# Performance work log

Measured on AMD Instinct MI355X. Metric: run time of the kernel, lower is better.

## Reference

```python
import jax, jax.numpy as jnp
import numpy as np

N = 100000   # nodes
E = 1600000  # edges per meta-path graph
D_IN = 256
H = 4        # num_heads
F = 32       # out_feats per head
D_HID = H * F  # 128
D_SEM = 128  # semantic attention hidden dim
C = 8        # output classes
NEG_SLOPE = 0.2


def setup_inputs() -> dict:
    key = jax.random.key(0)
    ks = jax.random.split(key, 24)
    inp = {
        "x": jax.random.normal(ks[0], (N, D_IN), dtype=jnp.float32),
        "src0": jax.random.randint(ks[1], (E,), 0, N),
        "dst0": jax.random.randint(ks[2], (E,), 0, N),
        "ew0": jax.random.uniform(ks[3], (E,), dtype=jnp.float32),
        "src1": jax.random.randint(ks[4], (E,), 0, N),
        "dst1": jax.random.randint(ks[5], (E,), 0, N),
        "ew1": jax.random.uniform(ks[6], (E,), dtype=jnp.float32),
    }
    s_in = 1.0 / np.sqrt(D_IN)
    s_f = 1.0 / np.sqrt(F)
    s_h = 1.0 / np.sqrt(D_HID)
    s_s = 1.0 / np.sqrt(D_SEM)
    # GAT params for meta-path 0 and 1 (tuple feat -> separate fc_src/fc_dst)
    inp["Wsrc0"] = jax.random.normal(ks[7], (D_IN, D_HID), dtype=jnp.float32) * s_in
    inp["Wdst0"] = jax.random.normal(ks[8], (D_IN, D_HID), dtype=jnp.float32) * s_in
    inp["al0"] = jax.random.normal(ks[9], (H, F), dtype=jnp.float32) * s_f
    inp["ar0"] = jax.random.normal(ks[10], (H, F), dtype=jnp.float32) * s_f
    inp["b0"] = jnp.zeros((D_HID,), dtype=jnp.float32)
    inp["Wsrc1"] = jax.random.normal(ks[11], (D_IN, D_HID), dtype=jnp.float32) * s_in
    inp["Wdst1"] = jax.random.normal(ks[12], (D_IN, D_HID), dtype=jnp.float32) * s_in
    inp["al1"] = jax.random.normal(ks[13], (H, F), dtype=jnp.float32) * s_f
    inp["ar1"] = jax.random.normal(ks[14], (H, F), dtype=jnp.float32) * s_f
    inp["b1"] = jnp.zeros((D_HID,), dtype=jnp.float32)
    # Semantic attention: Linear(D_HID->128) -> tanh -> Linear(128->1, no bias)
    inp["Wp1"] = jax.random.normal(ks[15], (D_HID, D_SEM), dtype=jnp.float32) * s_h
    inp["bp1"] = jnp.zeros((D_SEM,), dtype=jnp.float32)
    inp["Wp2"] = jax.random.normal(ks[16], (D_SEM, 1), dtype=jnp.float32) * s_s
    # Prediction head
    inp["Wo"] = jax.random.normal(ks[17], (D_HID, C), dtype=jnp.float32) * s_h
    inp["bo"] = jnp.zeros((C,), dtype=jnp.float32)
    return inp


def gat_conv(x, Wsrc, Wdst, al, ar, b, src, dst, ew):
    # feat_src/feat_dst: [N, H, F]
    fs = (x @ Wsrc).reshape(N, H, F)
    fd = (x @ Wdst).reshape(N, H, F)
    el = jnp.einsum('nhf,hf->nh', fs, al)  # [N, H]
    er = jnp.einsum('nhf,hf->nh', fd, ar)  # [N, H]
    e = jax.nn.leaky_relu(el[src] + er[dst], negative_slope=NEG_SLOPE)  # [E, H]
    a = jax.nn.sigmoid(e) * ew[:, None]  # [E, H]  (sigmoid attention * edge_weight)
    m = fs[src] * a[:, :, None]  # [E, H, F]
    out = jax.ops.segment_sum(m, dst, num_segments=N)  # [N, H, F]
    out = out + b.reshape(1, H, F)
    return jax.nn.elu(out).reshape(N, H * F)


def semantic_attention(z, Wp1, bp1, Wp2):
    # z: [N, P, D_HID]
    w = jnp.tanh(z @ Wp1 + bp1) @ Wp2  # [N, P, 1]
    w = w.mean(axis=0)                  # [P, 1]
    beta = jax.nn.softmax(w, axis=0)    # softmax over meta-paths
    return (beta[None] * z).sum(axis=1)  # [N, D_HID]


def reference(x, src0, dst0, ew0, src1, dst1, ew1,
              Wsrc0, Wdst0, al0, ar0, b0,
              Wsrc1, Wdst1, al1, ar1, b1,
              Wp1, bp1, Wp2, Wo, bo):
    z0 = gat_conv(x, Wsrc0, Wdst0, al0, ar0, b0, src0, dst0, ew0)
    z1 = gat_conv(x, Wsrc1, Wdst1, al1, ar1, b1, src1, dst1, ew1)
    z = jnp.stack([z0, z1], axis=1)  # [N, 2, H*F]
    h = semantic_attention(z, Wp1, bp1, Wp2)  # [N, H*F]
    return h @ Wo + bo  # [N, C]
```

## Files before the change

kernel.cpp:

```cpp
#include <hip/hip_runtime.h>
#include <hip/hip_fp16.h>
#include <math.h>

#define N_NODES 100000
#define N_EDGES 1600000
#define D_IN    256
#define D_HID   128
#define NH      4
#define NF      32
#define D_SEM   128
#define NC      8
#define NEG_SLOPE 0.2f
#define BUCKET  64
#define BIN_SHIFT 8
#define BINS    391
#define BIN_CAP 4608
#define CHUNK   4096

typedef _Float16 half8 __attribute__((ext_vector_type(8)));
typedef float    floatx4 __attribute__((ext_vector_type(4)));

__global__ void prep_fold(const float* __restrict__ Ws0, const float* __restrict__ al0,
                          const float* __restrict__ Wd0, const float* __restrict__ ar0,
                          const float* __restrict__ Ws1, const float* __restrict__ al1,
                          const float* __restrict__ Wd1, const float* __restrict__ ar1,
                          float* __restrict__ WF) {
    int d = threadIdx.x;
    for (int p = 0; p < 2; ++p) {
        const float* Ws = p ? Ws1 : Ws0;
        const float* al = p ? al1 : al0;
        const float* Wd = p ? Wd1 : Wd0;
        const float* ar = p ? ar1 : ar0;
        for (int h = 0; h < NH; ++h) {
            float se = 0.f, sr = 0.f;
            for (int f = 0; f < NF; ++f) {
                se = fmaf(Ws[d*D_HID + h*NF + f], al[h*NF + f], se);
                sr = fmaf(Wd[d*D_HID + h*NF + f], ar[h*NF + f], sr);
            }
            WF[d*16 + p*8 + h]     = se;
            WF[d*16 + p*8 + 4 + h] = sr;
        }
    }
}

__global__ __launch_bounds__(256) void prep_tr(const float* __restrict__ Ws0,
                                               const float* __restrict__ Ws1,
                                               const float* __restrict__ Wp1,
                                               __half* __restrict__ WT0,
                                               __half* __restrict__ WT1,
                                               __half* __restrict__ WP1T) {
    int g = blockIdx.x * 256 + threadIdx.x;
    if (g < 32768) {
        int c = g >> 8, k = g & 255;
        WT0[g] = __float2half_rn(Ws0[k*D_HID + c]);
    } else if (g < 65536) {
        int g2 = g - 32768;
        int c = g2 >> 8, k = g2 & 255;
        WT1[g2] = __float2half_rn(Ws1[k*D_HID + c]);
    } else {
        int g2 = g - 65536;
        int c = g2 >> 7, k = g2 & 127;
        WP1T[g2] = __float2half_rn(Wp1[k*D_SEM + c]);
    }
}

__global__ __launch_bounds__(256) void er_el_kernel(const float* __restrict__ x,
                                                    const float* __restrict__ WF,
                                                    float* __restrict__ eler,
                                                    __half* __restrict__ XH) {
    __shared__ float xs[16][260];
    __shared__ float wfs[4096];
    int tid = threadIdx.x;
    #pragma unroll
    for (int i = 0; i < 16; ++i) wfs[tid + i*256] = WF[tid + i*256];
    int n0 = blockIdx.x * 16;
    #pragma unroll
    for (int i = 0; i < 4; ++i) {
        int id = tid + i*256;
        int r = id >> 6, c = (id & 63) << 2;
        *(float4*)&xs[r][c] = *(const float4*)&x[(size_t)(n0 + r)*D_IN + c];
    }
    __syncthreads();
    int node = tid >> 4, c = tid & 15;
    float s = 0.f;
    #pragma unroll 8
    for (int k = 0; k < 256; ++k) s = fmaf(xs[node][k], wfs[k*16 + c], s);
    int p = c >> 3, e = (c >> 2) & 1, h = c & 3;
    eler[(p*2 + e)*400000 + (n0 + node)*4 + h] = s;

    #pragma unroll
    for (int i = 0; i < 4; ++i) {
        int id = tid + i*256;
        int r = id >> 6, c4 = (id & 63) << 2;
        float4 v = *(const float4*)&xs[r][c4];
        __half2 h0 = __floats2half2_rn(v.x, v.y);
        __half2 h1 = __floats2half2_rn(v.z, v.w);
        uint2 pk; pk.x = *(unsigned*)&h0; pk.y = *(unsigned*)&h1;
        *(uint2*)&XH[(size_t)(n0 + r)*D_IN + c4] = pk;
    }
}

__global__ __launch_bounds__(256) void gemm_fs_mfma(const __half* __restrict__ XH,
                                                    const __half* __restrict__ WT,
                                                    __half* __restrict__ FS) {
    __shared__ unsigned short xs[64][64];
    __shared__ unsigned short ws[128][64];
    int tid = threadIdx.x;
    int row0 = blockIdx.x * 64;
    int wid = tid >> 6, lane = tid & 63;
    int wm = wid >> 1, wn = wid & 1;
    int lr = lane & 15, lk = lane >> 4;

    floatx4 acc[2][4];
    #pragma unroll
    for (int m = 0; m < 2; ++m)
        #pragma unroll
        for (int n = 0; n < 4; ++n) acc[m][n] = (floatx4){0.f, 0.f, 0.f, 0.f};

    for (int k0 = 0; k0 < D_IN; k0 += 64) {
        #pragma unroll
        for (int i = 0; i < 2; ++i) {
            int id = tid + i*256;
            int r = id >> 3, c8 = (id & 7) << 3;
            int grow = row0 + r;
            uint4 pk = make_uint4(0u, 0u, 0u, 0u);
            if (grow < N_NODES) pk = *(const uint4*)&XH[(size_t)grow*D_IN + k0 + c8];
            int cc = (((c8 >> 3) ^ (r & 7)) << 3);
            *(uint4*)&xs[r][cc] = pk;
        }
        #pragma unroll
        for (int i = 0; i < 8; ++i) {
            int id = tid + i*256;
            int col = id >> 4, c4 = (id & 15) << 2;
            uint2 pk = *(const uint2*)&WT[col*256 + k0 + c4];
            int cc = (((c4 >> 3) ^ (col & 7)) << 3) + (c4 & 7);
            *(uint2*)&ws[col][cc] = pk;
        }
        __syncthreads();
        #pragma unroll
        for (int kk = 0; kk < 2; ++kk) {
            int ksub = kk*4 + lk;
            half8 a[2], b[4];
            #pragma unroll
            for (int m = 0; m < 2; ++m) {
                int r = wm*32 + m*16 + lr;
                a[m] = *(half8*)&xs[r][((ksub ^ (r & 7)) << 3)];
            }
            #pragma unroll
            for (int n = 0; n < 4; ++n) {
                int c = wn*64 + n*16 + lr;
                b[n] = *(half8*)&ws[c][((ksub ^ (c & 7)) << 3)];
            }
            #pragma unroll
            for (int m = 0; m < 2; ++m)
                #pragma unroll
                for (int n = 0; n < 4; ++n)
                    acc[m][n] = __builtin_amdgcn_mfma_f32_16x16x32_f16(a[m], b[n], acc[m][n], 0, 0, 0);
        }
        __syncthreads();
    }

    unsigned short* outs = &ws[0][0];
    #pragma unroll
    for (int m = 0; m < 2; ++m)
        #pragma unroll
        for (int n = 0; n < 4; ++n) {
            int col = wn*64 + n*16 + lr;
            #pragma unroll
            for (int r4 = 0; r4 < 4; ++r4) {
                int rr = wm*32 + m*16 + lk*4 + r4;
                __half hv = __float2half_rn(acc[m][n][r4]);
                outs[rr*128 + col] = *(unsigned short*)&hv;
            }
        }
    __syncthreads();
    #pragma unroll
    for (int i = 0; i < 8; ++i) {
        int id = tid + i*256;
        int r = id >> 5, c4 = (id & 31) << 2;
        int grow = row0 + r;
        if (grow < N_NODES)
            *(uint2*)&FS[(size_t)grow*D_HID + c4] = *(uint2*)&outs[r*128 + c4];
    }
}

__global__ __launch_bounds__(1024) void bin_kernel(const int* __restrict__ src,
                                                   const int* __restrict__ dst,
                                                   const float* __restrict__ ew,
                                                   int* __restrict__ gcur,
                                                   uint2* __restrict__ binned) {
    __shared__ uint2 stage[CHUNK];
    __shared__ unsigned short binof[CHUNK];
    __shared__ int bcnt[512], boff[512], gbase[512], brun[512];
    int tid = threadIdx.x;
    int c0 = blockIdx.x * CHUNK;
    int C = N_EDGES - c0; if (C > CHUNK) C = CHUNK;
    if (C <= 0) return;

    if (tid < 512) bcnt[tid] = 0;
    __syncthreads();
    for (int j = tid; j < C; j += 1024)
        atomicAdd(&bcnt[dst[c0 + j] >> BIN_SHIFT], 1);
    __syncthreads();

    int v = (tid < 512) ? bcnt[tid] : 0;
    if (tid < 512) boff[tid] = v;
    __syncthreads();
    for (int o = 1; o < 512; o <<= 1) {
        int u = (tid < 512 && tid >= o) ? boff[tid - o] : 0;
        __syncthreads();
        if (tid < 512) boff[tid] += u;
        __syncthreads();
    }
    if (tid < 512) {
        boff[tid] -= v;
        brun[tid] = 0;
        if (tid < BINS) gbase[tid] = v ? atomicAdd(&gcur[tid], v) : 0;
    }
    __syncthreads();

    for (int j = tid; j < C; j += 1024) {
        int e = c0 + j;
        int d = dst[e];
        int b = d >> BIN_SHIFT;
        unsigned q = (unsigned)(ew[e] * 32767.f + 0.5f);
        int p = atomicAdd(&brun[b], 1);
        int sl = boff[b] + p;
        stage[sl] = make_uint2(((unsigned)src[e] << 15) | q, (unsigned)d);
        binof[sl] = (unsigned short)b;
    }
    __syncthreads();

    for (int j = tid; j < C; j += 1024) {
        int b = binof[j];
        int off = gbase[b] + (j - boff[b]);
        if (off < BIN_CAP) binned[b * BIN_CAP + off] = stage[j];
    }
}

__global__ __launch_bounds__(1024) void bucket_kernel(const int* __restrict__ gcur,
                                                      const uint2* __restrict__ binned,
                                                      int* __restrict__ cnt,
                                                      unsigned* __restrict__ edg) {
    __shared__ unsigned buck[256 * BUCKET];
    __shared__ int lcnt[256];
    int tid = threadIdx.x;
    int b = blockIdx.x;
    int n0 = b << BIN_SHIFT;
    if (tid < 256) lcnt[tid] = 0;
    __syncthreads();

    int cE = gcur[b]; if (cE > BIN_CAP) cE = BIN_CAP;
    for (int j = tid; j < cE; j += 1024) {
        uint2 r = binned[b * BIN_CAP + j];
        int dl = (int)r.y - n0;
        int p = atomicAdd(&lcnt[dl], 1);
        if (p < BUCKET) buck[(dl << 6) + p] = r.x;
    }
    __syncthreads();

    const uint4* b4 = (const uint4*)buck;
    uint4* e4 = (uint4*)edg;
    for (int i = tid; i < 256 * BUCKET / 4; i += 1024) {
        int node = n0 + (i >> 4);
        int used = lcnt[i >> 4];
        if (node < N_NODES && ((i & 15) << 2) < used)
            e4[((size_t)node << 4) + (i & 15)] = b4[i];
    }
    if (tid < 256) {
        int node = n0 + tid;
        if (node < N_NODES) cnt[node] = lcnt[tid] < BUCKET ? lcnt[tid] : BUCKET;
    }
}

__device__ __forceinline__ float sel4(float4 v, int h) {
    float ab = (h & 1) ? v.y : v.x;
    float cd = (h & 1) ? v.w : v.z;
    return (h & 2) ? cd : ab;
}
__device__ __forceinline__ float coef_of(unsigned w, float v) {
    float a = (float)(w & 32767u) * (1.f / 32767.f);
    v = v > 0.f ? v : NEG_SLOPE * v;
    return a * __builtin_amdgcn_rcpf(1.f + __expf(-v));
}

__global__ __launch_bounds__(256) void agg_kernel(const __half* __restrict__ FS,
                                                  const float* __restrict__ el,
                                                  const float* __restrict__ er,
                                                  const int* __restrict__ cnt,
                                                  const unsigned* __restrict__ edg,
                                                  const float* __restrict__ bias,
                                                  __half* __restrict__ zh) {
    int wv = (blockIdx.x * 256 + threadIdx.x) >> 6;
    int lane = threadIdx.x & 63;
    if (wv >= N_NODES) return;
    int q   = lane >> 4;
    int ql  = lane & 15;
    int hh  = lane & 3;
    int eL  = lane >> 2;
    int cn = cnt[wv];
    if (cn > BUCKET) cn = BUCKET;
    int beg = wv << 6;
    const __half* fsq = FS + (ql << 3);

    unsigned w0 = 0, w1 = 0, w2 = 0, w3 = 0;
    if (eL      < cn) w0 = edg[beg + eL];
    if (eL + 16 < cn) w1 = edg[beg + 16 + eL];
    if (eL + 32 < cn) w2 = edg[beg + 32 + eL];
    if (eL + 48 < cn) w3 = edg[beg + 48 + eL];
    int s0v = (int)(w0 >> 15), s1v = (int)(w1 >> 15);
    int s2v = (int)(w2 >> 15), s3v = (int)(w3 >> 15);
    float4 el0 = *(const float4*)&el[s0v*4];
    float4 el1 = *(const float4*)&el[s1v*4];
    float4 el2 = *(const float4*)&el[s2v*4];
    float4 el3 = *(const float4*)&el[s3v*4];
    float erh = sel4(*(const float4*)&er[wv*4], hh);
    float c0v = (eL      < cn) ? coef_of(w0, sel4(el0, hh) + erh) : 0.f;
    float c1v = (eL + 16 < cn) ? coef_of(w1, sel4(el1, hh) + erh) : 0.f;
    float c2v = (eL + 32 < cn) ? coef_of(w2, sel4(el2, hh) + erh) : 0.f;
    float c3v = (eL + 48 < cn) ? coef_of(w3, sel4(el3, hh) + erh) : 0.f;

    float4 a0 = make_float4(0.f,0.f,0.f,0.f);
    float4 a1 = make_float4(0.f,0.f,0.f,0.f);
    int qsh = q << 2, hsel = ql >> 2;

#define AGG_PHASE(SP, CP, BASE)                                               \
    if ((BASE) < cn) {                                                        \
        _Pragma("unroll")                                                     \
        for (int u = 0; u < 4; ++u) {                                         \
            int lsrc = (u << 4) | qsh;                                        \
            int ssrc = __shfl(SP, lsrc);                                      \
            float av = __shfl(CP, lsrc | hsel);                               \
            uint4 raw = make_uint4(0u,0u,0u,0u);                              \
            if ((BASE) + (u << 2) + q < cn)                                   \
                raw = *(const uint4*)&fsq[(size_t)ssrc * D_HID];              \
            float2 f0 = __half22float2(*(__half2*)&raw.x);                    \
            float2 f1 = __half22float2(*(__half2*)&raw.y);                    \
            float2 f2 = __half22float2(*(__half2*)&raw.z);                    \
            float2 f3 = __half22float2(*(__half2*)&raw.w);                    \
            a0.x = fmaf(f0.x, av, a0.x); a0.y = fmaf(f0.y, av, a0.y);         \
            a0.z = fmaf(f1.x, av, a0.z); a0.w = fmaf(f1.y, av, a0.w);         \
            a1.x = fmaf(f2.x, av, a1.x); a1.y = fmaf(f2.y, av, a1.y);         \
            a1.z = fmaf(f3.x, av, a1.z); a1.w = fmaf(f3.y, av, a1.w);         \
        }                                                                     \
    }
    AGG_PHASE(s0v, c0v, 0)
    AGG_PHASE(s1v, c1v, 16)
    AGG_PHASE(s2v, c2v, 32)
    AGG_PHASE(s3v, c3v, 48)
#undef AGG_PHASE

    #pragma unroll
    for (int o = 16; o < 64; o <<= 1) {
        a0.x += __shfl_xor(a0.x, o); a0.y += __shfl_xor(a0.y, o);
        a0.z += __shfl_xor(a0.z, o); a0.w += __shfl_xor(a0.w, o);
        a1.x += __shfl_xor(a1.x, o); a1.y += __shfl_xor(a1.y, o);
        a1.z += __shfl_xor(a1.z, o); a1.w += __shfl_xor(a1.w, o);
    }

    if (q < 2) {
        int c = (ql << 3) + (q << 2);
        float4 r = q ? a1 : a0;
        float4 bv = *(const float4*)&bias[c];
        r.x += bv.x; r.y += bv.y; r.z += bv.z; r.w += bv.w;
        r.x = r.x > 0.f ? r.x : expm1f(r.x);
        r.y = r.y > 0.f ? r.y : expm1f(r.y);
        r.z = r.z > 0.f ? r.z : expm1f(r.z);
        r.w = r.w > 0.f ? r.w : expm1f(r.w);
        __half2 h0 = __floats2half2_rn(r.x, r.y);
        __half2 h1 = __floats2half2_rn(r.z, r.w);
        uint2 pk; pk.x = *(unsigned*)&h0; pk.y = *(unsigned*)&h1;
        *(uint2*)&zh[(size_t)wv*D_HID + c] = pk;
    }
}

__global__ __launch_bounds__(256) void sem_mfma(const __half* __restrict__ zh0,
                                                const __half* __restrict__ zh1,
                                                const __half* __restrict__ WP1T,
                                                const float* __restrict__ bp1,
                                                const float* __restrict__ Wp2,
                                                float* __restrict__ wsum) {
    __shared__ unsigned short zs[64][128];
    __shared__ unsigned short ps[128][128];
    __shared__ float red[4];
    const __half* z = blockIdx.y ? zh1 : zh0;
    int tid = threadIdx.x;
    int row0 = blockIdx.x * 64;
    int wid = tid >> 6, lane = tid & 63;
    int wm = wid >> 1, wn = wid & 1;
    int lr = lane & 15, lk = lane >> 4;

    #pragma unroll
    for (int i = 0; i < 4; ++i) {
        int id = tid + i*256;
        int r = id >> 4, ch = id & 15;
        int grow = row0 + r;
        uint4 pk = make_uint4(0u, 0u, 0u, 0u);
        if (grow < N_NODES) pk = *(const uint4*)&z[(size_t)grow*D_HID + (ch << 3)];
        *(uint4*)&zs[r][((ch ^ (r & 7)) << 3)] = pk;
    }
    #pragma unroll
    for (int i = 0; i < 16; ++i) {
        int id = tid + i*256;
        int c = id >> 5, k4 = (id & 31) << 2;
        uint2 pk = *(const uint2*)&WP1T[c*128 + k4];
        int cc = (((k4 >> 3) ^ (c & 7)) << 3) + (k4 & 7);
        *(uint2*)&ps[c][cc] = pk;
    }
    __syncthreads();

    floatx4 acc[2][4];
    #pragma unroll
    for (int m = 0; m < 2; ++m)
        #pragma unroll
        for (int n = 0; n < 4; ++n) acc[m][n] = (floatx4){0.f, 0.f, 0.f, 0.f};

    #pragma unroll
    for (int kk = 0; kk < 4; ++kk) {
        int ksub = kk*4 + lk;
        half8 a[2], b[4];
        #pragma unroll
        for (int m = 0; m < 2; ++m) {
            int r = wm*32 + m*16 + lr;
            a[m] = *(half8*)&zs[r][((ksub ^ (r & 7)) << 3)];
        }
        #pragma unroll
        for (int n = 0; n < 4; ++n) {
            int c = wn*64 + n*16 + lr;
            b[n] = *(half8*)&ps[c][((ksub ^ (c & 7)) << 3)];
        }
        #pragma unroll
        for (int m = 0; m < 2; ++m)
            #pragma unroll
            for (int n = 0; n < 4; ++n)
                acc[m][n] = __builtin_amdgcn_mfma_f32_16x16x32_f16(a[m], b[n], acc[m][n], 0, 0, 0);
    }

    float s = 0.f;
    #pragma unroll
    for (int m = 0; m < 2; ++m)
        #pragma unroll
        for (int n = 0; n < 4; ++n) {
            int col = wn*64 + n*16 + lr;
            float bp = bp1[col];
            float w2 = Wp2[col];
            #pragma unroll
            for (int r4 = 0; r4 < 4; ++r4) {
                int grow = row0 + wm*32 + m*16 + lk*4 + r4;
                if (grow < N_NODES) {
                    float v = acc[m][n][r4] + bp;
                    float t = 1.f - 2.f / (__expf(2.f*v) + 1.f);
                    s = fmaf(t, w2, s);
                }
            }
        }
    #pragma unroll
    for (int o = 1; o < 64; o <<= 1) s += __shfl_xor(s, o);
    if (lane == 0) red[wid] = s;
    __syncthreads();
    if (tid == 0) atomicAdd(&wsum[blockIdx.y], red[0] + red[1] + red[2] + red[3]);
}

__global__ __launch_bounds__(256) void final_kernel(const __half* __restrict__ zh0,
                                                    const __half* __restrict__ zh1,
                                                    const float* __restrict__ Wo,
                                                    const float* __restrict__ bo,
                                                    const float* __restrict__ wsum,
                                                    float* __restrict__ out) {
    __shared__ float z0s[32][132];
    __shared__ float z1s[32][132];
    __shared__ float wos[128*8];
    __shared__ float bos[8];
    int tid = threadIdx.x;
    int n0 = blockIdx.x * 32;
    #pragma unroll
    for (int i = 0; i < 4; ++i) wos[tid + i*256] = Wo[tid + i*256];
    if (tid < 8) bos[tid] = bo[tid];
    #pragma unroll
    for (int i = 0; i < 2; ++i) {
        int id = tid + i*256;
        int r = id >> 4, c8 = (id & 15) << 3;
        uint4 p0 = *(const uint4*)&zh0[(size_t)(n0 + r)*D_HID + c8];
        uint4 p1 = *(const uint4*)&zh1[(size_t)(n0 + r)*D_HID + c8];
        float2 q0 = __half22float2(*(__half2*)&p0.x);
        float2 q1 = __half22float2(*(__half2*)&p0.y);
        float2 q2 = __half22float2(*(__half2*)&p0.z);
        float2 q3 = __half22float2(*(__half2*)&p0.w);
        *(float4*)&z0s[r][c8]     = make_float4(q0.x, q0.y, q1.x, q1.y);
        *(float4*)&z0s[r][c8 + 4] = make_float4(q2.x, q2.y, q3.x, q3.y);
        q0 = __half22float2(*(__half2*)&p1.x);
        q1 = __half22float2(*(__half2*)&p1.y);
        q2 = __half22float2(*(__half2*)&p1.z);
        q3 = __half22float2(*(__half2*)&p1.w);
        *(float4*)&z1s[r][c8]     = make_float4(q0.x, q0.y, q1.x, q1.y);
        *(float4*)&z1s[r][c8 + 4] = make_float4(q2.x, q2.y, q3.x, q3.y);
    }
    __syncthreads();

    float w0 = wsum[0] * (1.f / N_NODES), w1 = wsum[1] * (1.f / N_NODES);
    float m = fmaxf(w0, w1);
    float e0 = __expf(w0 - m), e1 = __expf(w1 - m);
    float b0 = e0 / (e0 + e1), b1 = 1.f - b0;

    int node = tid >> 3, c = tid & 7;
    float s = bos[c];
    #pragma unroll 8
    for (int k = 0; k < 128; ++k) {
        float hk = b0 * z0s[node][k] + b1 * z1s[node][k];
        s = fmaf(hk, wos[k*8 + c], s);
    }
    out[(n0 + node)*NC + c] = s;
}

extern "C" void kernel_launch(void* const* d_in, const int* in_sizes, int n_in,
                              void* d_out, int out_size, void* d_ws, size_t ws_size,
                              hipStream_t stream) {
    const float* x     = (const float*)d_in[0];
    const int*   src0  = (const int*)  d_in[1];
    const int*   dst0  = (const int*)  d_in[2];
    const float* ew0   = (const float*)d_in[3];
    const int*   src1  = (const int*)  d_in[4];
    const int*   dst1  = (const int*)  d_in[5];
    const float* ew1   = (const float*)d_in[6];
    const float* Wsrc0 = (const float*)d_in[7];
    const float* Wdst0 = (const float*)d_in[8];
    const float* al0   = (const float*)d_in[9];
    const float* ar0   = (const float*)d_in[10];
    const float* b0    = (const float*)d_in[11];
    const float* Wsrc1 = (const float*)d_in[12];
    const float* Wdst1 = (const float*)d_in[13];
    const float* al1   = (const float*)d_in[14];
    const float* ar1   = (const float*)d_in[15];
    const float* b1    = (const float*)d_in[16];
    const float* Wp1   = (const float*)d_in[17];
    const float* bp1   = (const float*)d_in[18];
    const float* Wp2   = (const float*)d_in[19];
    const float* Wo    = (const float*)d_in[20];
    const float* bo    = (const float*)d_in[21];
    float* out = (float*)d_out;

    float*    ws     = (float*)d_ws;
    __half*   FS     = (__half*)ws;
    __half*   ZH0    = (__half*)(ws + 6400000);
    __half*   ZH1    = (__half*)(ws + 12800000);
    __half*   XH     = (__half*)(ws + 19200000);
    float*    ELER   = ws + 32000000;
    float*    WF     = ELER + 1600000;
    float*    WSUM   = WF + 4096;
    __half*   WT0    = (__half*)(WSUM + 8);
    __half*   WT1    = (__half*)((float*)WT0 + 16384);
    __half*   WP1T   = (__half*)((float*)WT1 + 16384);
    int*      CNT0   = (int*)((float*)WP1T + 8192);
    int*      CNT1   = CNT0  + 100000;
    int*      GCUR0  = CNT1  + 100000;
    int*      GCUR1  = GCUR0 + 512;
    unsigned* EDG    = (unsigned*)(GCUR1 + 512);
    uint2*    BINNED = (uint2*)(EDG + 6400000);

    hipMemsetAsync(GCUR0, 0, sizeof(int)*1024, stream);
    hipMemsetAsync(WSUM, 0, sizeof(float)*4, stream);

    prep_fold<<<1, 256, 0, stream>>>(Wsrc0, al0, Wdst0, ar0, Wsrc1, al1, Wdst1, ar1, WF);
    prep_tr<<<320, 256, 0, stream>>>(Wsrc0, Wsrc1, Wp1, WT0, WT1, WP1T);
    er_el_kernel<<<N_NODES/16, 256, 0, stream>>>(x, WF, ELER, XH);

    bin_kernel<<<(N_EDGES + CHUNK - 1)/CHUNK, 1024, 0, stream>>>(src0, dst0, ew0, GCUR0, BINNED);
    bucket_kernel<<<BINS, 1024, 0, stream>>>(GCUR0, BINNED, CNT0, EDG);
    gemm_fs_mfma<<<(N_NODES + 63)/64, 256, 0, stream>>>(XH, WT0, FS);
    agg_kernel<<<(N_NODES*64)/256, 256, 0, stream>>>(FS, ELER, ELER + 400000, CNT0, EDG, b0, ZH0);

    bin_kernel<<<(N_EDGES + CHUNK - 1)/CHUNK, 1024, 0, stream>>>(src1, dst1, ew1, GCUR1, BINNED);
    bucket_kernel<<<BINS, 1024, 0, stream>>>(GCUR1, BINNED, CNT1, EDG);
    gemm_fs_mfma<<<(N_NODES + 63)/64, 256, 0, stream>>>(XH, WT1, FS);
    agg_kernel<<<(N_NODES*64)/256, 256, 0, stream>>>(FS, ELER + 800000, ELER + 1200000, CNT1, EDG, b1, ZH1);

    dim3 semgrid((N_NODES + 63)/64, 2);
    sem_mfma<<<semgrid, 256, 0, stream>>>(ZH0, ZH1, WP1T, bp1, Wp2, WSUM);
    final_kernel<<<N_NODES/32, 256, 0, stream>>>(ZH0, ZH1, Wo, bo, WSUM, out);
}
```

Measured before the change: 610.7 us.

## Replace two-pass binned edge bucketing with direct global-atomic scatter

Removes the bin_kernel/bucket_kernel pair, which staged edges through shared memory and a global binned buffer, and replaces it with a single grid-stride kernel that does a global atomicAdd on each destination's count and writes the packed edge record straight into its 64-slot bucket. The aim is to drop one kernel launch and the intermediate binned round trip per meta-path. In exchange it relies on heavily contended global atomics and scattered 4-byte writes. Edge order within a bucket becomes nondeterministic, which can change floating-point summation order. The aggregation kernel also switches from float4 loads plus select to scalar loads of the el/er entries.

```diff
diff --git a/kernel.cpp b/kernel.cpp
--- a/kernel.cpp
+++ b/kernel.cpp
@@ -12,10 +12,6 @@
 #define NC      8
 #define NEG_SLOPE 0.2f
 #define BUCKET  64
-#define BIN_SHIFT 8
-#define BINS    391
-#define BIN_CAP 4608
-#define CHUNK   4096
 
 typedef _Float16 half8 __attribute__((ext_vector_type(8)));
 typedef float    floatx4 __attribute__((ext_vector_type(4)));
@@ -184,100 +180,22 @@
     }
 }
 
-__global__ __launch_bounds__(1024) void bin_kernel(const int* __restrict__ src,
-                                                   const int* __restrict__ dst,
-                                                   const float* __restrict__ ew,
-                                                   int* __restrict__ gcur,
-                                                   uint2* __restrict__ binned) {
-    __shared__ uint2 stage[CHUNK];
-    __shared__ unsigned short binof[CHUNK];
-    __shared__ int bcnt[512], boff[512], gbase[512], brun[512];
-    int tid = threadIdx.x;
-    int c0 = blockIdx.x * CHUNK;
-    int C = N_EDGES - c0; if (C > CHUNK) C = CHUNK;
-    if (C <= 0) return;
-
-    if (tid < 512) bcnt[tid] = 0;
-    __syncthreads();
-    for (int j = tid; j < C; j += 1024)
-        atomicAdd(&bcnt[dst[c0 + j] >> BIN_SHIFT], 1);
-    __syncthreads();
-
-    int v = (tid < 512) ? bcnt[tid] : 0;
-    if (tid < 512) boff[tid] = v;
-    __syncthreads();
-    for (int o = 1; o < 512; o <<= 1) {
-        int u = (tid < 512 && tid >= o) ? boff[tid - o] : 0;
-        __syncthreads();
-        if (tid < 512) boff[tid] += u;
-        __syncthreads();
-    }
-    if (tid < 512) {
-        boff[tid] -= v;
-        brun[tid] = 0;
-        if (tid < BINS) gbase[tid] = v ? atomicAdd(&gcur[tid], v) : 0;
-    }
-    __syncthreads();
-
-    for (int j = tid; j < C; j += 1024) {
-        int e = c0 + j;
-        int d = dst[e];
-        int b = d >> BIN_SHIFT;
-        unsigned q = (unsigned)(ew[e] * 32767.f + 0.5f);
-        int p = atomicAdd(&brun[b], 1);
-        int sl = boff[b] + p;
-        stage[sl] = make_uint2(((unsigned)src[e] << 15) | q, (unsigned)d);
-        binof[sl] = (unsigned short)b;
-    }
-    __syncthreads();
-
-    for (int j = tid; j < C; j += 1024) {
-        int b = binof[j];
-        int off = gbase[b] + (j - boff[b]);
-        if (off < BIN_CAP) binned[b * BIN_CAP + off] = stage[j];
-    }
-}
-
-__global__ __launch_bounds__(1024) void bucket_kernel(const int* __restrict__ gcur,
-                                                      const uint2* __restrict__ binned,
+__global__ __launch_bounds__(256) void scatter_kernel(const int* __restrict__ src,
+                                                      const int* __restrict__ dst,
+                                                      const float* __restrict__ ew,
                                                       int* __restrict__ cnt,
                                                       unsigned* __restrict__ edg) {
-    __shared__ unsigned buck[256 * BUCKET];
-    __shared__ int lcnt[256];
-    int tid = threadIdx.x;
-    int b = blockIdx.x;
-    int n0 = b << BIN_SHIFT;
-    if (tid < 256) lcnt[tid] = 0;
-    __syncthreads();
-
-    int cE = gcur[b]; if (cE > BIN_CAP) cE = BIN_CAP;
-    for (int j = tid; j < cE; j += 1024) {
-        uint2 r = binned[b * BIN_CAP + j];
-        int dl = (int)r.y - n0;
-        int p = atomicAdd(&lcnt[dl], 1);
-        if (p < BUCKET) buck[(dl << 6) + p] = r.x;
-    }
-    __syncthreads();
-
-    const uint4* b4 = (const uint4*)buck;
-    uint4* e4 = (uint4*)edg;
-    for (int i = tid; i < 256 * BUCKET / 4; i += 1024) {
-        int node = n0 + (i >> 4);
-        int used = lcnt[i >> 4];
-        if (node < N_NODES && ((i & 15) << 2) < used)
-            e4[((size_t)node << 4) + (i & 15)] = b4[i];
-    }
-    if (tid < 256) {
-        int node = n0 + tid;
-        if (node < N_NODES) cnt[node] = lcnt[tid] < BUCKET ? lcnt[tid] : BUCKET;
-    }
-}
-
-__device__ __forceinline__ float sel4(float4 v, int h) {
-    float ab = (h & 1) ? v.y : v.x;
-    float cd = (h & 1) ? v.w : v.z;
-    return (h & 2) ? cd : ab;
-}
+    int i = blockIdx.x * 256 + threadIdx.x;
+    int stride = gridDim.x * 256;
+    for (int e = i; e < N_EDGES; e += stride) {
+        int d = dst[e];
+        unsigned q = (unsigned)(ew[e] * 32767.f + 0.5f);
+        unsigned rec = ((unsigned)src[e] << 15) | q;
+        int pos = atomicAdd(&cnt[d], 1);
+        if (pos < BUCKET) edg[((size_t)d << 6) + pos] = rec;
+    }
+}
+
 __device__ __forceinline__ float coef_of(unsigned w, float v) {
     float a = (float)(w & 32767u) * (1.f / 32767.f);
     v = v > 0.f ? v : NEG_SLOPE * v;
@@ -310,15 +228,15 @@
     if (eL + 48 < cn) w3 = edg[beg + 48 + eL];
     int s0v = (int)(w0 >> 15), s1v = (int)(w1 >> 15);
     int s2v = (int)(w2 >> 15), s3v = (int)(w3 >> 15);
-    float4 el0 = *(const float4*)&el[s0v*4];
-    float4 el1 = *(const float4*)&el[s1v*4];
-    float4 el2 = *(const float4*)&el[s2v*4];
-    float4 el3 = *(const float4*)&el[s3v*4];
-    float erh = sel4(*(const float4*)&er[wv*4], hh);
-    float c0v = (eL      < cn) ? coef_of(w0, sel4(el0, hh) + erh) : 0.f;
-    float c1v = (eL + 16 < cn) ? coef_of(w1, sel4(el1, hh) + erh) : 0.f;
-    float c2v = (eL + 32 < cn) ? coef_of(w2, sel4(el2, hh) + erh) : 0.f;
-    float c3v = (eL + 48 < cn) ? coef_of(w3, sel4(el3, hh) + erh) : 0.f;
+    float el0 = el[s0v*4 + hh];
+    float el1 = el[s1v*4 + hh];
+    float el2 = el[s2v*4 + hh];
+    float el3 = el[s3v*4 + hh];
+    float erh = er[wv*4 + hh];
+    float c0v = (eL      < cn) ? coef_of(w0, el0 + erh) : 0.f;
+    float c1v = (eL + 16 < cn) ? coef_of(w1, el1 + erh) : 0.f;
+    float c2v = (eL + 32 < cn) ? coef_of(w2, el2 + erh) : 0.f;
+    float c3v = (eL + 48 < cn) ? coef_of(w3, el3 + erh) : 0.f;
 
     float4 a0 = make_float4(0.f,0.f,0.f,0.f);
     float4 a1 = make_float4(0.f,0.f,0.f,0.f);
@@ -552,25 +470,20 @@
     __half*   WP1T   = (__half*)((float*)WT1 + 16384);
     int*      CNT0   = (int*)((float*)WP1T + 8192);
     int*      CNT1   = CNT0  + 100000;
-    int*      GCUR0  = CNT1  + 100000;
-    int*      GCUR1  = GCUR0 + 512;
-    unsigned* EDG    = (unsigned*)(GCUR1 + 512);
-    uint2*    BINNED = (uint2*)(EDG + 6400000);
-
-    hipMemsetAsync(GCUR0, 0, sizeof(int)*1024, stream);
+    unsigned* EDG    = (unsigned*)(CNT1 + 100000);
+
+    hipMemsetAsync(CNT0, 0, sizeof(int)*200000, stream);
     hipMemsetAsync(WSUM, 0, sizeof(float)*4, stream);
 
     prep_fold<<<1, 256, 0, stream>>>(Wsrc0, al0, Wdst0, ar0, Wsrc1, al1, Wdst1, ar1, WF);
     prep_tr<<<320, 256, 0, stream>>>(Wsrc0, Wsrc1, Wp1, WT0, WT1, WP1T);
     er_el_kernel<<<N_NODES/16, 256, 0, stream>>>(x, WF, ELER, XH);
 
-    bin_kernel<<<(N_EDGES + CHUNK - 1)/CHUNK, 1024, 0, stream>>>(src0, dst0, ew0, GCUR0, BINNED);
-    bucket_kernel<<<BINS, 1024, 0, stream>>>(GCUR0, BINNED, CNT0, EDG);
+    scatter_kernel<<<2048, 256, 0, stream>>>(src0, dst0, ew0, CNT0, EDG);
     gemm_fs_mfma<<<(N_NODES + 63)/64, 256, 0, stream>>>(XH, WT0, FS);
     agg_kernel<<<(N_NODES*64)/256, 256, 0, stream>>>(FS, ELER, ELER + 400000, CNT0, EDG, b0, ZH0);
 
-    bin_kernel<<<(N_EDGES + CHUNK - 1)/CHUNK, 1024, 0, stream>>>(src1, dst1, ew1, GCUR1, BINNED);
-    bucket_kernel<<<BINS, 1024, 0, stream>>>(GCUR1, BINNED, CNT1, EDG);
+    scatter_kernel<<<2048, 256, 0, stream>>>(src1, dst1, ew1, CNT1, EDG);
     gemm_fs_mfma<<<(N_NODES + 63)/64, 256, 0, stream>>>(XH, WT1, FS);
     agg_kernel<<<(N_NODES*64)/256, 256, 0, stream>>>(FS, ELER + 800000, ELER + 1200000, CNT1, EDG, b1, ZH1);
 
```

Result: slower. 729.7 us (+19.5%).
